# Performance work log

Hardware: AMD Instinct MI355X
Metric: run time of the kernel (lower is better)

Reference implementation:

```python
import jax, jax.numpy as jnp
import numpy as np

B, T, I, H, C = 512, 256, 128, 64, 3  # batch, seq_len, input_size, hidden_size, num_classes


def _lstm_dir(x, w_ih, w_hh, b, reverse):
    """Single-direction LSTM over x: (B, T, D_in) -> (B, T, H).

    Gate order matches PyTorch: i, f, g, o. b = b_ih + b_hh (combined).
    Input-to-gate GEMM is hoisted out of the scan for efficiency.
    """
    xg = jnp.einsum('bti,gi->btg', x, w_ih) + b  # (B, T, 4H)
    if reverse:
        xg = xg[:, ::-1]
    xg_t = jnp.swapaxes(xg, 0, 1)  # (T, B, 4H)
    h0 = jnp.zeros((x.shape[0], w_hh.shape[1]), x.dtype)
    c0 = jnp.zeros_like(h0)

    def step(carry, g):
        h, c = carry
        g = g + h @ w_hh.T
        i, f, gg, o = jnp.split(g, 4, axis=-1)
        i = jax.nn.sigmoid(i)
        f = jax.nn.sigmoid(f)
        gg = jnp.tanh(gg)
        o = jax.nn.sigmoid(o)
        c = f * c + i * gg
        h = o * jnp.tanh(c)
        return (h, c), h

    _, hs = jax.lax.scan(step, (h0, c0), xg_t)  # (T, B, H)
    hs = jnp.swapaxes(hs, 0, 1)  # (B, T, H)
    if reverse:
        hs = hs[:, ::-1]
    return hs


def setup_inputs() -> dict:
    key = jax.random.key(0)
    ks = jax.random.split(key, 20)
    s = 1.0 / np.sqrt(H)  # PyTorch LSTM init scale
    d = {"x": jax.random.normal(ks[0], (B, T, I), dtype=jnp.float32)}
    i = 1
    for l, d_in in [(0, I), (1, 2 * H)]:
        for suf in ["f", "r"]:
            d[f"w_ih_l{l}{suf}"] = jax.random.uniform(ks[i], (4 * H, d_in), minval=-s, maxval=s); i += 1
            d[f"w_hh_l{l}{suf}"] = jax.random.uniform(ks[i], (4 * H, H), minval=-s, maxval=s); i += 1
            d[f"b_l{l}{suf}"] = jax.random.uniform(ks[i], (4 * H,), minval=-s, maxval=s); i += 1
    d["fc_w"] = jax.random.uniform(ks[i], (C, 2 * H), minval=-s, maxval=s); i += 1
    d["fc_b"] = jax.random.uniform(ks[i], (C,), minval=-s, maxval=s)
    return d


def reference(x, w_ih_l0f, w_hh_l0f, b_l0f, w_ih_l0r, w_hh_l0r, b_l0r,
              w_ih_l1f, w_hh_l1f, b_l1f, w_ih_l1r, w_hh_l1r, b_l1r,
              fc_w, fc_b):
    # Layer 0 (bidirectional)
    h0f = _lstm_dir(x, w_ih_l0f, w_hh_l0f, b_l0f, False)
    h0r = _lstm_dir(x, w_ih_l0r, w_hh_l0r, b_l0r, True)
    x1 = jnp.concatenate([h0f, h0r], axis=-1)  # (B, T, 2H)
    # (inter-layer dropout is identity in eval mode)
    # Layer 1 (bidirectional)
    h1f = _lstm_dir(x1, w_ih_l1f, w_hh_l1f, b_l1f, False)
    h1r = _lstm_dir(x1, w_ih_l1r, w_hh_l1r, b_l1r, True)
    out = jnp.concatenate([h1f, h1r], axis=-1)  # (B, T, 2H)
    last = out[:, -1, :]  # (B, 2H); dropout is identity in eval mode
    return last @ fc_w.T + fc_b  # (B, C) logits
```

## Files before the change

kernel.cpp:

```cpp
#include <hip/hip_runtime.h>

#define TT 256
#define BB 512
#define NG 256
#define KIN 128

typedef _Float16 half2v __attribute__((ext_vector_type(2)));
typedef _Float16 half4v __attribute__((ext_vector_type(4)));
typedef _Float16 half8v __attribute__((ext_vector_type(8)));
typedef float float4v __attribute__((ext_vector_type(4)));

__device__ __forceinline__ float sigmoid_(float x){ return 1.f/(1.f+__expf(-x)); }
__device__ __forceinline__ float tanh_(float x){
  float xc = fminf(fmaxf(x,-9.f),9.f);
  float e = __expf(2.f*xc);
  return (e-1.f)/(e+1.f);
}

#if __has_builtin(__builtin_amdgcn_fdot2)
__device__ __forceinline__ float fdot2_(half2v a, half2v b, float c){
  return __builtin_amdgcn_fdot2(a, b, c, false);
}
#else
__device__ __forceinline__ float fdot2_(half2v a, half2v b, float c){
  return c + (float)a[0]*(float)b[0] + (float)a[1]*(float)b[1];
}
#endif

__device__ __forceinline__ half4v ld4h(const float* p){
  float4v v = *reinterpret_cast<const float4v*>(p);
  half4v h; h[0]=(_Float16)v[0]; h[1]=(_Float16)v[1]; h[2]=(_Float16)v[2]; h[3]=(_Float16)v[3];
  return h;
}

__global__ __launch_bounds__(256)
void conv_weights(const float* __restrict__ s0, const float* __restrict__ s1,
                  const float* __restrict__ s2, const float* __restrict__ s3,
                  const float* __restrict__ s4, const float* __restrict__ s5,
                  _Float16* __restrict__ dst)
{
  const int bid = blockIdx.x, tid = threadIdx.x;
  const float* src; int off, idx;
  if (bid < 128)      { src=s0; off=0;      idx=bid*256+tid; }
  else if (bid < 256) { src=s1; off=32768;  idx=(bid-128)*256+tid; }
  else if (bid < 384) { src=s2; off=65536;  idx=(bid-256)*256+tid; }
  else if (bid < 448) { src=s3; off=98304;  idx=(bid-384)*256+tid; }
  else if (bid < 512) { src=s4; off=114688; idx=(bid-448)*256+tid; }
  else                { src=s5; off=131072; idx=(bid-512)*256+tid; }
  dst[off+idx] = (_Float16)src[idx];
}

template<typename AT>
__global__ __launch_bounds__(256)
void gemm_xg(const AT* __restrict__ A, const _Float16* __restrict__ W16,
             const float* __restrict__ bias, _Float16* __restrict__ Cout)
{
  __shared__ __align__(16) _Float16 aL[64][72];
  __shared__ __align__(16) _Float16 wL[256][72];
  const int tid  = threadIdx.x;
  const int wave = tid >> 6;
  const int lane = tid & 63;
  const int lr   = lane & 15;
  const int kg   = lane >> 4;
  const size_t m0 = (size_t)blockIdx.x * 64;

  float4v acc[4][4];
  #pragma unroll
  for (int a=0;a<4;a++)
    #pragma unroll
    for (int b=0;b<4;b++)
      acc[a][b] = float4v{0.f,0.f,0.f,0.f};

  for (int kc = 0; kc < KIN; kc += 64) {
    if constexpr (__is_same(AT, float)) {
      #pragma unroll
      for (int q=0;q<4;q++){
        int fi = tid + q*256;
        int r = fi >> 4, c4 = (fi & 15)*4;
        *reinterpret_cast<half4v*>(&aL[r][c4]) = ld4h(&A[(m0+(size_t)r)*KIN + kc + c4]);
      }
    } else {
      #pragma unroll
      for (int q=0;q<2;q++){
        int fi = tid + q*256;
        int r = fi >> 3, c8 = (fi & 7)*8;
        *reinterpret_cast<half8v*>(&aL[r][c8]) =
            *reinterpret_cast<const half8v*>(&A[(m0+(size_t)r)*KIN + kc + c8]);
      }
    }
    #pragma unroll
    for (int q=0;q<8;q++){
      int fi = tid + q*256;
      int n = fi >> 3, c8 = (fi & 7)*8;
      *reinterpret_cast<half8v*>(&wL[n][c8]) =
          *reinterpret_cast<const half8v*>(&W16[(size_t)n*KIN + kc + c8]);
    }
    __syncthreads();
    #pragma unroll
    for (int ks=0; ks<64; ks+=32){
      half8v af[4], bf[4];
      #pragma unroll
      for (int rt=0;rt<4;rt++)
        af[rt] = *reinterpret_cast<const half8v*>(&aL[rt*16+lr][ks + kg*8]);
      #pragma unroll
      for (int ct=0;ct<4;ct++)
        bf[ct] = *reinterpret_cast<const half8v*>(&wL[wave*64 + ct*16 + lr][ks + kg*8]);
      #pragma unroll
      for (int rt=0;rt<4;rt++)
        #pragma unroll
        for (int ct=0;ct<4;ct++)
          acc[rt][ct] = __builtin_amdgcn_mfma_f32_16x16x32_f16(af[rt], bf[ct], acc[rt][ct], 0,0,0);
    }
    __syncthreads();
  }
  #pragma unroll
  for (int ct=0;ct<4;ct++){
    const int col = wave*64 + ct*16 + lr;
    const float bv = bias[col];
    #pragma unroll
    for (int rt=0;rt<4;rt++){
      const size_t rbase = m0 + rt*16 + kg*4;
      #pragma unroll
      for (int i=0;i<4;i++)
        Cout[(rbase+(size_t)i)*NG + col] = (_Float16)(acc[rt][ct][i] + bv);
    }
  }
}

template<int MODE>
__global__ __launch_bounds__(128)
void lstm_scan(const _Float16* __restrict__ xgF, const _Float16* __restrict__ xgR,
               int gridF,
               const _Float16* __restrict__ whhF, const _Float16* __restrict__ whhR,
               _Float16* __restrict__ x1out, float* __restrict__ hfin)
{
  const int tid = threadIdx.x;
  const bool rev = (int)blockIdx.x >= gridF;
  const int b = rev ? ((int)blockIdx.x - gridF) : (int)blockIdx.x;
  const _Float16* __restrict__ xg  = rev ? xgR : xgF;
  const _Float16* __restrict__ whh = rev ? whhR : whhF;
  const int g0 = tid;
  const int g1 = tid + 128;

  __shared__ __align__(16) _Float16 h16[64];
  __shared__ __align__(16) float act2[64][2];

  half2v w0[32], w1[32];
  #pragma unroll
  for (int q=0;q<8;q++){
    *reinterpret_cast<half8v*>(&w0[q*4]) =
        *reinterpret_cast<const half8v*>(&whh[(size_t)g0*64 + q*8]);
    *reinterpret_cast<half8v*>(&w1[q*4]) =
        *reinterpret_cast<const half8v*>(&whh[(size_t)g1*64 + q*8]);
  }
  if (tid < 64) h16[tid] = (_Float16)0.f;
  float c_r = 0.f, h_last = 0.f;
  __syncthreads();

  const _Float16* __restrict__ xgb = xg + (size_t)b*TT*NG;
  const int t0 = rev ? TT-1 : 0;
  const int t1 = rev ? TT-2 : 1;
  float curA = (float)xgb[(size_t)t0*NG + g0];
  float curB = (float)xgb[(size_t)t0*NG + g1];
  float nxA  = (float)xgb[(size_t)t1*NG + g0];
  float nxB  = (float)xgb[(size_t)t1*NG + g1];

  for (int tt=0; tt<TT; ++tt){
    const int t   = rev ? (TT-1-tt) : tt;
    const int tnn = (tt+2 < TT) ? (tt+2) : (TT-1);
    const int tp  = rev ? (TT-1-tnn) : tnn;
    float pfA = (float)xgb[(size_t)tp*NG + g0];
    float pfB = (float)xgb[(size_t)tp*NG + g1];

    float a0=0.f, b0=0.f, a1=0.f, b1=0.f;
    #pragma unroll
    for (int q=0;q<8;q++){
      half2v hh[4];
      *reinterpret_cast<half8v*>(&hh[0]) = *reinterpret_cast<const half8v*>(&h16[q*8]);
      a0 = fdot2_(w0[q*4+0], hh[0], a0);
      b0 = fdot2_(w0[q*4+1], hh[1], b0);
      a0 = fdot2_(w0[q*4+2], hh[2], a0);
      b0 = fdot2_(w0[q*4+3], hh[3], b0);
      a1 = fdot2_(w1[q*4+0], hh[0], a1);
      b1 = fdot2_(w1[q*4+1], hh[1], b1);
      a1 = fdot2_(w1[q*4+2], hh[2], a1);
      b1 = fdot2_(w1[q*4+3], hh[3], b1);
    }
    const float pre0 = curA + (a0 + b0);
    const float pre1 = curB + (a1 + b1);

    if (tid >= 64){
      act2[tid-64][0] = sigmoid_(pre0);
      act2[tid-64][1] = sigmoid_(pre1);
    }
    float iv = 0.f, gv = 0.f;
    if (tid < 64){
      iv = sigmoid_(pre0);
      gv = tanh_(pre1);
    }
    __syncthreads();
    if (tid < 64){
      const float fv = act2[tid][0], ov = act2[tid][1];
      c_r = fv*c_r + iv*gv;
      const float h = ov * tanh_(c_r);
      h_last = h;
      h16[tid] = (_Float16)h;
      if constexpr (MODE==0)
        x1out[((size_t)b*TT + t)*128 + (rev ? 64 : 0) + tid] = (_Float16)h;
    }
    __syncthreads();
    curA = nxA; curB = nxB; nxA = pfA; nxB = pfB;
  }
  if constexpr (MODE==1){
    if (tid < 64) hfin[(size_t)b*64 + tid] = h_last;
  }
}

__global__ __launch_bounds__(256)
void final_fuse(const _Float16* __restrict__ x1, const float* __restrict__ w_ih,
                const float* __restrict__ bvec, const float* __restrict__ hfin,
                const float* __restrict__ fcw, const float* __restrict__ fcb,
                float* __restrict__ out)
{
  const int b = blockIdx.x, tid = threadIdx.x;
  __shared__ float xs[128];
  __shared__ float act[256];
  __shared__ float hall[128];
  if (tid < 128) xs[tid] = (float)x1[((size_t)b*TT + (TT-1))*128 + tid];
  __syncthreads();
  float a = bvec[tid];
  #pragma unroll
  for (int kk=0;kk<32;kk++){
    float4v wv = *reinterpret_cast<const float4v*>(&w_ih[(size_t)tid*128 + kk*4]);
    a += wv[0]*xs[kk*4] + wv[1]*xs[kk*4+1] + wv[2]*xs[kk*4+2] + wv[3]*xs[kk*4+3];
  }
  const int grp = tid>>6;
  act[tid] = (grp==2) ? tanh_(a) : sigmoid_(a);
  __syncthreads();
  if (tid < 64) {
    float c = act[tid]*act[128+tid];
    float h = act[192+tid]*tanh_(c);
    hall[64+tid] = h;
    hall[tid] = hfin[(size_t)b*64 + tid];
  }
  __syncthreads();
  if (tid < 3) {
    float acc2 = fcb[tid];
    for (int k=0;k<128;k++) acc2 += fcw[(size_t)tid*128 + k]*hall[k];
    out[(size_t)b*3 + tid] = acc2;
  }
}

extern "C" void kernel_launch(void* const* d_in, const int* in_sizes, int n_in,
                              void* d_out, int out_size, void* d_ws, size_t ws_size,
                              hipStream_t stream) {
  const float* x        = (const float*)d_in[0];
  const float* w_ih_l0f = (const float*)d_in[1];
  const float* w_hh_l0f = (const float*)d_in[2];
  const float* b_l0f    = (const float*)d_in[3];
  const float* w_ih_l0r = (const float*)d_in[4];
  const float* w_hh_l0r = (const float*)d_in[5];
  const float* b_l0r    = (const float*)d_in[6];
  const float* w_ih_l1f = (const float*)d_in[7];
  const float* w_hh_l1f = (const float*)d_in[8];
  const float* b_l1f    = (const float*)d_in[9];
  const float* w_ih_l1r = (const float*)d_in[10];
  const float* b_l1r    = (const float*)d_in[12];
  const float* fc_w     = (const float*)d_in[13];
  const float* fc_b     = (const float*)d_in[14];
  float* out = (float*)d_out;

  const size_t XG_BYTES = (size_t)BB*TT*NG*2;
  const size_t X1_BYTES = (size_t)BB*TT*128*2;
  const size_t HF_BYTES = (size_t)BB*64*4;
  const size_t W16_BYTES = (size_t)147456*2;
  if (ws_size < 2*XG_BYTES + X1_BYTES + HF_BYTES + W16_BYTES) return;
  _Float16* xgF  = (_Float16*)d_ws;
  _Float16* xgR  = (_Float16*)((char*)d_ws + XG_BYTES);
  _Float16* x1   = (_Float16*)((char*)d_ws + 2*XG_BYTES);
  float*    hfin = (float*)   ((char*)d_ws + 2*XG_BYTES + X1_BYTES);
  _Float16* w16  = (_Float16*)((char*)d_ws + 2*XG_BYTES + X1_BYTES + HF_BYTES);
  _Float16* wih_l0f16 = w16;
  _Float16* wih_l0r16 = w16 + 32768;
  _Float16* wih_l1f16 = w16 + 65536;
  _Float16* whh_l0f16 = w16 + 98304;
  _Float16* whh_l0r16 = w16 + 114688;
  _Float16* whh_l1f16 = w16 + 131072;

  const int MBLK = (BB*TT)/64;

  conv_weights<<<576, 256, 0, stream>>>(w_ih_l0f, w_ih_l0r, w_ih_l1f,
                                        w_hh_l0f, w_hh_l0r, w_hh_l1f, w16);
  gemm_xg<float><<<MBLK, 256, 0, stream>>>(x, wih_l0f16, b_l0f, xgF);
  gemm_xg<float><<<MBLK, 256, 0, stream>>>(x, wih_l0r16, b_l0r, xgR);
  lstm_scan<0><<<1024, 128, 0, stream>>>(xgF, xgR, 512, whh_l0f16, whh_l0r16, x1, nullptr);
  gemm_xg<_Float16><<<MBLK, 256, 0, stream>>>(x1, wih_l1f16, b_l1f, xgF);
  lstm_scan<1><<<512, 128, 0, stream>>>(xgF, nullptr, 512, whh_l1f16, nullptr, nullptr, hfin);
  final_fuse<<<BB, 256, 0, stream>>>(x1, w_ih_l1r, b_l1r, hfin, fc_w, fc_b, out);
}
```

Before: 489.5 us.

## Run LSTM scan as one wavefront per sequence computing all four gates per lane

The recurrent scan kernel now uses a single 64-lane wave per (batch, direction). Each lane holds all four gate weight rows for its hidden unit and computes i/f/g/o itself. This removes the shared-memory gate exchange and both block barriers per timestep. In exchange each lane does twice the dot-product work and holds more weight registers, and it relies on in-wave LDS ordering for the h vector. Tanh is also rewritten as a sigmoid-based form without clamping.

```diff
diff --git a/kernel.cpp b/kernel.cpp
--- a/kernel.cpp
+++ b/kernel.cpp
@@ -10,12 +10,8 @@
 typedef _Float16 half8v __attribute__((ext_vector_type(8)));
 typedef float float4v __attribute__((ext_vector_type(4)));
 
-__device__ __forceinline__ float sigmoid_(float x){ return 1.f/(1.f+__expf(-x)); }
-__device__ __forceinline__ float tanh_(float x){
-  float xc = fminf(fmaxf(x,-9.f),9.f);
-  float e = __expf(2.f*xc);
-  return (e-1.f)/(e+1.f);
-}
+__device__ __forceinline__ float sig_(float x){ return 1.f/(1.f+__expf(-x)); }
+__device__ __forceinline__ float th_(float x){ return fmaf(2.f, 1.f/(1.f+__expf(-2.f*x)), -1.f); }
 
 #if __has_builtin(__builtin_amdgcn_fdot2)
 __device__ __forceinline__ float fdot2_(half2v a, half2v b, float c){
@@ -128,92 +124,85 @@
 }
 
 template<int MODE>
-__global__ __launch_bounds__(128)
-void lstm_scan(const _Float16* __restrict__ xgF, const _Float16* __restrict__ xgR,
-               int gridF,
-               const _Float16* __restrict__ whhF, const _Float16* __restrict__ whhR,
-               _Float16* __restrict__ x1out, float* __restrict__ hfin)
-{
-  const int tid = threadIdx.x;
-  const bool rev = (int)blockIdx.x >= gridF;
-  const int b = rev ? ((int)blockIdx.x - gridF) : (int)blockIdx.x;
+__global__ __launch_bounds__(64)
+void lstm_scan_w1(const _Float16* __restrict__ xgF, const _Float16* __restrict__ xgR,
+                  int nF,
+                  const _Float16* __restrict__ whhF, const _Float16* __restrict__ whhR,
+                  _Float16* __restrict__ x1out, float* __restrict__ hfin)
+{
+  const int j = threadIdx.x;
+  const bool rev = (int)blockIdx.x >= nF;
+  const int b = rev ? ((int)blockIdx.x - nF) : (int)blockIdx.x;
   const _Float16* __restrict__ xg  = rev ? xgR : xgF;
   const _Float16* __restrict__ whh = rev ? whhR : whhF;
-  const int g0 = tid;
-  const int g1 = tid + 128;
-
-  __shared__ __align__(16) _Float16 h16[64];
-  __shared__ __align__(16) float act2[64][2];
-
-  half2v w0[32], w1[32];
+
+  __shared__ __align__(16) _Float16 hs[64];
+
+  half2v wi[32], wf[32], wg[32], wo[32];
   #pragma unroll
   for (int q=0;q<8;q++){
-    *reinterpret_cast<half8v*>(&w0[q*4]) =
-        *reinterpret_cast<const half8v*>(&whh[(size_t)g0*64 + q*8]);
-    *reinterpret_cast<half8v*>(&w1[q*4]) =
-        *reinterpret_cast<const half8v*>(&whh[(size_t)g1*64 + q*8]);
-  }
-  if (tid < 64) h16[tid] = (_Float16)0.f;
-  float c_r = 0.f, h_last = 0.f;
+    *reinterpret_cast<half8v*>(&wi[q*4]) = *reinterpret_cast<const half8v*>(&whh[(size_t)(      j)*64 + q*8]);
+    *reinterpret_cast<half8v*>(&wf[q*4]) = *reinterpret_cast<const half8v*>(&whh[(size_t)( 64 + j)*64 + q*8]);
+    *reinterpret_cast<half8v*>(&wg[q*4]) = *reinterpret_cast<const half8v*>(&whh[(size_t)(128 + j)*64 + q*8]);
+    *reinterpret_cast<half8v*>(&wo[q*4]) = *reinterpret_cast<const half8v*>(&whh[(size_t)(192 + j)*64 + q*8]);
+  }
+  hs[j] = (_Float16)0.f;
+  float c = 0.f, h_last = 0.f;
   __syncthreads();
 
   const _Float16* __restrict__ xgb = xg + (size_t)b*TT*NG;
-  const int t0 = rev ? TT-1 : 0;
-  const int t1 = rev ? TT-2 : 1;
-  float curA = (float)xgb[(size_t)t0*NG + g0];
-  float curB = (float)xgb[(size_t)t0*NG + g1];
-  float nxA  = (float)xgb[(size_t)t1*NG + g0];
-  float nxB  = (float)xgb[(size_t)t1*NG + g1];
+  const int tA = rev ? (TT-1) : 0;
+  const int tB = rev ? (TT-2) : 1;
+  float cur[4], nx[4];
+  #pragma unroll
+  for (int g=0; g<4; ++g){
+    cur[g] = (float)xgb[(size_t)tA*NG + g*64 + j];
+    nx[g]  = (float)xgb[(size_t)tB*NG + g*64 + j];
+  }
 
   for (int tt=0; tt<TT; ++tt){
     const int t   = rev ? (TT-1-tt) : tt;
     const int tnn = (tt+2 < TT) ? (tt+2) : (TT-1);
     const int tp  = rev ? (TT-1-tnn) : tnn;
-    float pfA = (float)xgb[(size_t)tp*NG + g0];
-    float pfB = (float)xgb[(size_t)tp*NG + g1];
-
-    float a0=0.f, b0=0.f, a1=0.f, b1=0.f;
-    #pragma unroll
-    for (int q=0;q<8;q++){
-      half2v hh[4];
-      *reinterpret_cast<half8v*>(&hh[0]) = *reinterpret_cast<const half8v*>(&h16[q*8]);
-      a0 = fdot2_(w0[q*4+0], hh[0], a0);
-      b0 = fdot2_(w0[q*4+1], hh[1], b0);
-      a0 = fdot2_(w0[q*4+2], hh[2], a0);
-      b0 = fdot2_(w0[q*4+3], hh[3], b0);
-      a1 = fdot2_(w1[q*4+0], hh[0], a1);
-      b1 = fdot2_(w1[q*4+1], hh[1], b1);
-      a1 = fdot2_(w1[q*4+2], hh[2], a1);
-      b1 = fdot2_(w1[q*4+3], hh[3], b1);
-    }
-    const float pre0 = curA + (a0 + b0);
-    const float pre1 = curB + (a1 + b1);
-
-    if (tid >= 64){
-      act2[tid-64][0] = sigmoid_(pre0);
-      act2[tid-64][1] = sigmoid_(pre1);
-    }
-    float iv = 0.f, gv = 0.f;
-    if (tid < 64){
-      iv = sigmoid_(pre0);
-      gv = tanh_(pre1);
-    }
-    __syncthreads();
-    if (tid < 64){
-      const float fv = act2[tid][0], ov = act2[tid][1];
-      c_r = fv*c_r + iv*gv;
-      const float h = ov * tanh_(c_r);
-      h_last = h;
-      h16[tid] = (_Float16)h;
-      if constexpr (MODE==0)
-        x1out[((size_t)b*TT + t)*128 + (rev ? 64 : 0) + tid] = (_Float16)h;
-    }
-    __syncthreads();
-    curA = nxA; curB = nxB; nxA = pfA; nxB = pfB;
-  }
-  if constexpr (MODE==1){
-    if (tid < 64) hfin[(size_t)b*64 + tid] = h_last;
-  }
+    float pf[4];
+    #pragma unroll
+    for (int g=0; g<4; ++g) pf[g] = (float)xgb[(size_t)tp*NG + g*64 + j];
+
+    half2v h2[32];
+    #pragma unroll
+    for (int q=0;q<8;q++)
+      *reinterpret_cast<half8v*>(&h2[q*4]) = *reinterpret_cast<const half8v*>(&hs[q*8]);
+
+    float ai=0.f, a2i=0.f, af=0.f, a2f=0.f, ag=0.f, a2g=0.f, ao=0.f, a2o=0.f;
+    #pragma unroll
+    for (int q=0;q<16;q++){
+      half2v hA = h2[2*q], hB = h2[2*q+1];
+      ai  = fdot2_(wi[2*q],   hA, ai);
+      a2i = fdot2_(wi[2*q+1], hB, a2i);
+      af  = fdot2_(wf[2*q],   hA, af);
+      a2f = fdot2_(wf[2*q+1], hB, a2f);
+      ag  = fdot2_(wg[2*q],   hA, ag);
+      a2g = fdot2_(wg[2*q+1], hB, a2g);
+      ao  = fdot2_(wo[2*q],   hA, ao);
+      a2o = fdot2_(wo[2*q+1], hB, a2o);
+    }
+    const float iv = sig_(cur[0] + (ai + a2i));
+    const float fv = sig_(cur[1] + (af + a2f));
+    const float gv = th_ (cur[2] + (ag + a2g));
+    const float ov = sig_(cur[3] + (ao + a2o));
+
+    c = fv*c + iv*gv;
+    const float h = ov * th_(c);
+    h_last = h;
+    hs[j] = (_Float16)h;
+    if constexpr (MODE==0)
+      x1out[((size_t)b*TT + t)*128 + (rev ? 64 : 0) + j] = (_Float16)h;
+
+    #pragma unroll
+    for (int g=0; g<4; ++g){ cur[g] = nx[g]; nx[g] = pf[g]; }
+  }
+  if constexpr (MODE==1)
+    hfin[(size_t)b*64 + j] = h_last;
 }
 
 __global__ __launch_bounds__(256)
@@ -235,11 +224,11 @@
     a += wv[0]*xs[kk*4] + wv[1]*xs[kk*4+1] + wv[2]*xs[kk*4+2] + wv[3]*xs[kk*4+3];
   }
   const int grp = tid>>6;
-  act[tid] = (grp==2) ? tanh_(a) : sigmoid_(a);
+  act[tid] = (grp==2) ? th_(a) : sig_(a);
   __syncthreads();
   if (tid < 64) {
     float c = act[tid]*act[128+tid];
-    float h = act[192+tid]*tanh_(c);
+    float h = act[192+tid]*th_(c);
     hall[64+tid] = h;
     hall[tid] = hfin[(size_t)b*64 + tid];
   }
@@ -293,8 +282,8 @@
                                         w_hh_l0f, w_hh_l0r, w_hh_l1f, w16);
   gemm_xg<float><<<MBLK, 256, 0, stream>>>(x, wih_l0f16, b_l0f, xgF);
   gemm_xg<float><<<MBLK, 256, 0, stream>>>(x, wih_l0r16, b_l0r, xgR);
-  lstm_scan<0><<<1024, 128, 0, stream>>>(xgF, xgR, 512, whh_l0f16, whh_l0r16, x1, nullptr);
+  lstm_scan_w1<0><<<1024, 64, 0, stream>>>(xgF, xgR, 512, whh_l0f16, whh_l0r16, x1, nullptr);
   gemm_xg<_Float16><<<MBLK, 256, 0, stream>>>(x1, wih_l1f16, b_l1f, xgF);
-  lstm_scan<1><<<512, 128, 0, stream>>>(xgF, nullptr, 512, whh_l1f16, nullptr, nullptr, hfin);
+  lstm_scan_w1<1><<<512, 64, 0, stream>>>(xgF, nullptr, 512, whh_l1f16, nullptr, nullptr, hfin);
   final_fuse<<<BB, 256, 0, stream>>>(x1, w_ih_l1r, b_l1r, hfin, fc_w, fc_b, out);
 }
```

After: 478.6 us. 2.2% less time.
